# Kernel optimization log

Measured on AMD Instinct MI355X. Metric: run time of the kernel, lower is better.

Reference implementation:

```python
import jax, jax.numpy as jnp
import numpy as np
import math

EPS = 1e-8


def _l2_normalize(v, axis=-1, eps=EPS):
    # Matches torch.nn.functional.normalize: v / max(||v||, eps)
    n = jnp.sqrt(jnp.sum(v * v, axis=axis, keepdims=True))
    return v / jnp.maximum(n, eps)


def _gelu_tanh(x):
    c = math.sqrt(2.0 / math.pi)
    return 0.5 * x * (1.0 + jnp.tanh(c * (x + 0.044715 * x * x * x)))


def setup_inputs() -> dict:
    key = jax.random.key(0)
    k1, k2, k3, k4 = jax.random.split(key, 4)
    B, T, D, K = 8, 4096, 2048, 8
    x = jax.random.normal(k1, (B, T, D), dtype=jnp.float32)
    # module initializes prototypes as normalized randn(K, D)
    P = jax.random.normal(k2, (K, D), dtype=jnp.float32)
    P = _l2_normalize(P)
    log_tau = jnp.asarray(math.log(2.0), dtype=jnp.float32)
    log_blend = jnp.asarray(math.log(0.3 / 0.7), dtype=jnp.float32)
    return {"x": x, "prototypes": P, "log_tau": log_tau, "log_blend": log_blend}


def reference(x, prototypes, log_tau, log_blend):
    tau = jnp.exp(log_tau)
    alpha = jax.nn.sigmoid(log_blend)
    B, T, D = x.shape
    x_norm = _l2_normalize(x)                      # (B, T, D)
    p_norm = _l2_normalize(prototypes)             # (K, D)
    sims = jnp.einsum('btd,kd->btk', x_norm, p_norm)  # tiny K=8 matmul
    sims = jnp.clip(sims, -1.0, 1.0)
    min_dist = jnp.min(1.0 - sims, axis=-1)        # (B, T)
    min_dist = jnp.clip(min_dist, 0.0, 2.0)
    novelty = 1.0 - jnp.exp(-tau * min_dist)       # (B, T)
    scale = 1.0 - alpha + alpha * novelty[..., None]
    scale = jnp.clip(scale, 0.1, 10.0)
    return _gelu_tanh(x * scale)
```

## Files before the change

### kernel.cpp

```cpp
#include <hip/hip_runtime.h>
#include <math.h>

#define D 2048
#define K 8
#define BLOCK 256
#define ROWS 2

typedef __fp16 h2 __attribute__((ext_vector_type(2)));

__device__ __forceinline__ float rcp_fast(float x) {
    return __builtin_amdgcn_rcpf(x);
}

#if __has_builtin(__builtin_amdgcn_fdot2)
#define FDOT2(a, b, c) __builtin_amdgcn_fdot2((a), (b), (c), false)
#else
__device__ __forceinline__ float fdot2_emul(h2 a, h2 b, float c) {
    return fmaf((float)a[0], (float)b[0], fmaf((float)a[1], (float)b[1], c));
}
#define FDOT2 fdot2_emul
#endif

__device__ __forceinline__ float gelu_tanh_fast(float y) {
    const float nc = -2.3022078977f;
    float w = y * fmaf(0.044715f, y * y, 1.0f);
    return y * rcp_fast(1.0f + exp2f(nc * w));
}

__device__ __forceinline__ float dot4(const float4& a, const float4& b) {
    return fmaf(a.w, b.w, fmaf(a.z, b.z, fmaf(a.y, b.y, a.x * b.x)));
}

#define FOLDSTEP(x, y, m)                                   \
    {                                                       \
        float _k = (lane & (m)) ? (y) : (x);                \
        float _o = (lane & (m)) ? (x) : (y);                \
        x = _k + __shfl_xor(_o, (m));                       \
    }

__global__ __launch_bounds__(BLOCK, 4)
void novelty_gelu_kernel(const float* __restrict__ x,
                         const float* __restrict__ P,
                         const float* __restrict__ plog_tau,
                         const float* __restrict__ plog_blend,
                         float* __restrict__ out,
                         int nrows)
{
    __shared__ float s_inv[K];
    __shared__ float redT[2][ROWS][12][4];

    const int tid  = threadIdx.x;
    const int wave = tid >> 6;
    const int lane = tid & 63;
    const int col  = tid * 8;

    for (int k = wave; k < K; k += 4) {
        const float* pr = P + k * D;
        float s = 0.f;
        #pragma unroll
        for (int j = 0; j < 8; ++j) {
            float4 p = *(const float4*)(pr + j * 256 + lane * 4);
            s += dot4(p, p);
        }
        #pragma unroll
        for (int m = 1; m < 64; m <<= 1) s += __shfl_xor(s, m);
        if (lane == 0) s_inv[k] = 1.0f / fmaxf(sqrtf(s), 1e-8f);
    }
    __syncthreads();

    h2 pf[K][4];
    #pragma unroll
    for (int k = 0; k < K; ++k) {
        const float inv = s_inv[k];
        float4 p0 = *(const float4*)(P + k * D + col);
        float4 p1 = *(const float4*)(P + k * D + col + 4);
        pf[k][0] = __builtin_amdgcn_cvt_pkrtz(p0.x * inv, p0.y * inv);
        pf[k][1] = __builtin_amdgcn_cvt_pkrtz(p0.z * inv, p0.w * inv);
        pf[k][2] = __builtin_amdgcn_cvt_pkrtz(p1.x * inv, p1.y * inv);
        pf[k][3] = __builtin_amdgcn_cvt_pkrtz(p1.z * inv, p1.w * inv);
    }

    const float tau   = __expf(plog_tau[0]);
    const float alpha = 1.0f / (1.0f + __expf(-plog_blend[0]));
    const float oma   = 1.0f - alpha;

    const int stride = gridDim.x * ROWS;
    int row = blockIdx.x * ROWS;
    int buf = 0;

    float4 a[ROWS][2], b[ROWS][2];
    if (row < nrows) {
        #pragma unroll
        for (int r = 0; r < ROWS; ++r) {
            const float* xr = x + (size_t)(row + r) * D + col;
            a[r][0] = *(const float4*)(xr);
            a[r][1] = *(const float4*)(xr + 4);
        }
    }

    while (row < nrows) {
        const int nr = row + stride;
        if (nr < nrows) {
            #pragma unroll
            for (int r = 0; r < ROWS; ++r) {
                const float* xn = x + (size_t)(nr + r) * D + col;
                b[r][0] = *(const float4*)(xn);
                b[r][1] = *(const float4*)(xn + 4);
            }
        }

        #pragma unroll
        for (int r = 0; r < ROWS; ++r) {
            h2 xh[4];
            xh[0] = __builtin_amdgcn_cvt_pkrtz(a[r][0].x, a[r][0].y);
            xh[1] = __builtin_amdgcn_cvt_pkrtz(a[r][0].z, a[r][0].w);
            xh[2] = __builtin_amdgcn_cvt_pkrtz(a[r][1].x, a[r][1].y);
            xh[3] = __builtin_amdgcn_cvt_pkrtz(a[r][1].z, a[r][1].w);

            float ssq = 0.f;
            float dt[K];
            #pragma unroll
            for (int k = 0; k < K; ++k) dt[k] = 0.f;
            #pragma unroll
            for (int i = 0; i < 4; ++i) {
                ssq = FDOT2(xh[i], xh[i], ssq);
                #pragma unroll
                for (int k = 0; k < K; ++k)
                    dt[k] = FDOT2(xh[i], pf[k][i], dt[k]);
            }

            FOLDSTEP(dt[0], dt[1], 1);
            FOLDSTEP(dt[2], dt[3], 1);
            FOLDSTEP(dt[4], dt[5], 1);
            FOLDSTEP(dt[6], dt[7], 1);
            FOLDSTEP(dt[0], dt[2], 2);
            FOLDSTEP(dt[4], dt[6], 2);
            FOLDSTEP(dt[0], dt[4], 4);
            float vd = dt[0];
            vd += __shfl_xor(vd, 8);
            vd += __shfl_xor(vd, 16);
            vd += __shfl_xor(vd, 32);

            #pragma unroll
            for (int m = 1; m < 64; m <<= 1) ssq += __shfl_xor(ssq, m);

            if (lane < 8)       redT[buf][r][lane][wave] = vd;
            else if (lane == 8) redT[buf][r][8][wave]    = ssq;
        }

        __syncthreads();

        #pragma unroll
        for (int r = 0; r < ROWS; ++r) {
            float4 qs = *(const float4*)&redT[buf][r][8][0];
            float tssq = (qs.x + qs.y) + (qs.z + qs.w);
            float dmax = -3.0e38f;
            #pragma unroll
            for (int k = 0; k < K; ++k) {
                float4 q = *(const float4*)&redT[buf][r][k][0];
                dmax = fmaxf(dmax, (q.x + q.y) + (q.z + q.w));
            }
            const float inv_nx = 1.0f / fmaxf(sqrtf(tssq), 1e-8f);
            float sim = fminf(1.0f, fmaxf(-1.0f, dmax * inv_nx));
            float md  = fminf(fmaxf(1.0f - sim, 0.0f), 2.0f);
            float scale = oma + alpha * (1.0f - __expf(-tau * md));
            scale = fminf(fmaxf(scale, 0.1f), 10.0f);

            float* outr = out + (size_t)(row + r) * D + col;
            float4 o0, o1;
            o0.x = gelu_tanh_fast(a[r][0].x * scale);
            o0.y = gelu_tanh_fast(a[r][0].y * scale);
            o0.z = gelu_tanh_fast(a[r][0].z * scale);
            o0.w = gelu_tanh_fast(a[r][0].w * scale);
            o1.x = gelu_tanh_fast(a[r][1].x * scale);
            o1.y = gelu_tanh_fast(a[r][1].y * scale);
            o1.z = gelu_tanh_fast(a[r][1].z * scale);
            o1.w = gelu_tanh_fast(a[r][1].w * scale);
            *(float4*)(outr)     = o0;
            *(float4*)(outr + 4) = o1;
        }

        #pragma unroll
        for (int r = 0; r < ROWS; ++r) { a[r][0] = b[r][0]; a[r][1] = b[r][1]; }
        row = nr;
        buf ^= 1;
    }
}

extern "C" void kernel_launch(void* const* d_in, const int* in_sizes, int n_in,
                              void* d_out, int out_size, void* d_ws, size_t ws_size,
                              hipStream_t stream) {
    const float* x  = (const float*)d_in[0];
    const float* P  = (const float*)d_in[1];
    const float* lt = (const float*)d_in[2];
    const float* lb = (const float*)d_in[3];
    float* out = (float*)d_out;

    const int nrows = in_sizes[0] / D;
    int grid = nrows / ROWS;
    if (grid > 2048) grid = 2048;

    novelty_gelu_kernel<<<grid, BLOCK, 0, stream>>>(x, P, lt, lb, out, nrows);
}
```

Baseline: 116.4 us.

## Split prototype norm into prelaunch kernel and use one-shot blocks per row pair

Prototype inverse norms move into a separate small kernel that writes to workspace. The persistent grid-stride loop with register double-buffering becomes a one-shot kernel launching one block per two rows. The final GELU now reads x from its fp16-packed copy instead of the fp32 values, so the input is rounded before the activation. This removes the per-block prototype norm recomputation and the loop overhead, but adds a second kernel launch, 16384 blocks that each reload the prototypes, and a loss of output precision.

Result: slower. 158.6 us (+36.3%).

```diff
diff --git a/kernel.cpp b/kernel.cpp
--- a/kernel.cpp
+++ b/kernel.cpp
@@ -39,151 +39,142 @@
     }
 
 __global__ __launch_bounds__(BLOCK, 4)
-void novelty_gelu_kernel(const float* __restrict__ x,
-                         const float* __restrict__ P,
-                         const float* __restrict__ plog_tau,
-                         const float* __restrict__ plog_blend,
-                         float* __restrict__ out,
-                         int nrows)
+void proto_norm_kernel(const float* __restrict__ P, float* __restrict__ invn)
 {
-    __shared__ float s_inv[K];
-    __shared__ float redT[2][ROWS][12][4];
+    __shared__ float part[4];
+    const int k    = blockIdx.x;
+    const int tid  = threadIdx.x;
+    const int wave = tid >> 6;
+    const int lane = tid & 63;
+
+    const float* pr = P + (size_t)k * D + tid * 8;
+    float4 p0 = *(const float4*)pr;
+    float4 p1 = *(const float4*)(pr + 4);
+    float s = dot4(p0, p0) + dot4(p1, p1);
+    #pragma unroll
+    for (int m = 1; m < 64; m <<= 1) s += __shfl_xor(s, m);
+    if (lane == 0) part[wave] = s;
+    __syncthreads();
+    if (tid == 0) {
+        float t = part[0] + part[1] + part[2] + part[3];
+        invn[k] = 1.0f / fmaxf(sqrtf(t), 1e-8f);
+    }
+}
+
+__global__ __launch_bounds__(BLOCK, 4)
+void novelty_gelu_oneshot(const float* __restrict__ x,
+                          const float* __restrict__ P,
+                          const float* __restrict__ invn,
+                          const float* __restrict__ plog_tau,
+                          const float* __restrict__ plog_blend,
+                          float* __restrict__ out,
+                          int nrows)
+{
+    __shared__ float redT[ROWS][9][4];
+    __shared__ float s_scale[ROWS];
 
     const int tid  = threadIdx.x;
     const int wave = tid >> 6;
     const int lane = tid & 63;
     const int col  = tid * 8;
+    const int r0   = blockIdx.x * ROWS;
 
-    for (int k = wave; k < K; k += 4) {
-        const float* pr = P + k * D;
-        float s = 0.f;
-        #pragma unroll
-        for (int j = 0; j < 8; ++j) {
-            float4 p = *(const float4*)(pr + j * 256 + lane * 4);
-            s += dot4(p, p);
-        }
-        #pragma unroll
-        for (int m = 1; m < 64; m <<= 1) s += __shfl_xor(s, m);
-        if (lane == 0) s_inv[k] = 1.0f / fmaxf(sqrtf(s), 1e-8f);
+    h2 xh[ROWS][4];
+    #pragma unroll
+    for (int r = 0; r < ROWS; ++r) {
+        const float* xr = x + (size_t)(r0 + r) * D + col;
+        float4 v0 = *(const float4*)(xr);
+        float4 v1 = *(const float4*)(xr + 4);
+        xh[r][0] = __builtin_amdgcn_cvt_pkrtz(v0.x, v0.y);
+        xh[r][1] = __builtin_amdgcn_cvt_pkrtz(v0.z, v0.w);
+        xh[r][2] = __builtin_amdgcn_cvt_pkrtz(v1.x, v1.y);
+        xh[r][3] = __builtin_amdgcn_cvt_pkrtz(v1.z, v1.w);
     }
-    __syncthreads();
 
     h2 pf[K][4];
     #pragma unroll
     for (int k = 0; k < K; ++k) {
-        const float inv = s_inv[k];
-        float4 p0 = *(const float4*)(P + k * D + col);
-        float4 p1 = *(const float4*)(P + k * D + col + 4);
+        const float inv = invn[k];
+        float4 p0 = *(const float4*)(P + (size_t)k * D + col);
+        float4 p1 = *(const float4*)(P + (size_t)k * D + col + 4);
         pf[k][0] = __builtin_amdgcn_cvt_pkrtz(p0.x * inv, p0.y * inv);
         pf[k][1] = __builtin_amdgcn_cvt_pkrtz(p0.z * inv, p0.w * inv);
         pf[k][2] = __builtin_amdgcn_cvt_pkrtz(p1.x * inv, p1.y * inv);
         pf[k][3] = __builtin_amdgcn_cvt_pkrtz(p1.z * inv, p1.w * inv);
     }
 
-    const float tau   = __expf(plog_tau[0]);
-    const float alpha = 1.0f / (1.0f + __expf(-plog_blend[0]));
-    const float oma   = 1.0f - alpha;
+    #pragma unroll
+    for (int r = 0; r < ROWS; ++r) {
+        float ssq = 0.f;
+        float dt[K];
+        #pragma unroll
+        for (int k = 0; k < K; ++k) dt[k] = 0.f;
+        #pragma unroll
+        for (int i = 0; i < 4; ++i) {
+            ssq = FDOT2(xh[r][i], xh[r][i], ssq);
+            #pragma unroll
+            for (int k = 0; k < K; ++k)
+                dt[k] = FDOT2(xh[r][i], pf[k][i], dt[k]);
+        }
 
-    const int stride = gridDim.x * ROWS;
-    int row = blockIdx.x * ROWS;
-    int buf = 0;
+        FOLDSTEP(dt[0], dt[1], 1);
+        FOLDSTEP(dt[2], dt[3], 1);
+        FOLDSTEP(dt[4], dt[5], 1);
+        FOLDSTEP(dt[6], dt[7], 1);
+        FOLDSTEP(dt[0], dt[2], 2);
+        FOLDSTEP(dt[4], dt[6], 2);
+        FOLDSTEP(dt[0], dt[4], 4);
+        float vd = dt[0];
+        vd += __shfl_xor(vd, 8);
+        vd += __shfl_xor(vd, 16);
+        vd += __shfl_xor(vd, 32);
 
-    float4 a[ROWS][2], b[ROWS][2];
-    if (row < nrows) {
         #pragma unroll
-        for (int r = 0; r < ROWS; ++r) {
-            const float* xr = x + (size_t)(row + r) * D + col;
-            a[r][0] = *(const float4*)(xr);
-            a[r][1] = *(const float4*)(xr + 4);
-        }
+        for (int m = 1; m < 64; m <<= 1) ssq += __shfl_xor(ssq, m);
+
+        if (lane < 8)       redT[r][lane][wave] = vd;
+        else if (lane == 8) redT[r][8][wave]    = ssq;
     }
 
-    while (row < nrows) {
-        const int nr = row + stride;
-        if (nr < nrows) {
-            #pragma unroll
-            for (int r = 0; r < ROWS; ++r) {
-                const float* xn = x + (size_t)(nr + r) * D + col;
-                b[r][0] = *(const float4*)(xn);
-                b[r][1] = *(const float4*)(xn + 4);
-            }
+    __syncthreads();
+
+    if (wave < ROWS) {
+        const int r = wave;
+        float4 qs = *(const float4*)&redT[r][8][0];
+        float tssq = (qs.x + qs.y) + (qs.z + qs.w);
+        float dmax = -3.0e38f;
+        #pragma unroll
+        for (int k = 0; k < K; ++k) {
+            float4 q = *(const float4*)&redT[r][k][0];
+            dmax = fmaxf(dmax, (q.x + q.y) + (q.z + q.w));
         }
+        const float tau   = __expf(plog_tau[0]);
+        const float alpha = 1.0f / (1.0f + __expf(-plog_blend[0]));
+        const float inv_nx = 1.0f / fmaxf(sqrtf(tssq), 1e-8f);
+        float sim = fminf(1.0f, fmaxf(-1.0f, dmax * inv_nx));
+        float md  = fminf(fmaxf(1.0f - sim, 0.0f), 2.0f);
+        float scale = (1.0f - alpha) + alpha * (1.0f - __expf(-tau * md));
+        scale = fminf(fmaxf(scale, 0.1f), 10.0f);
+        if (lane == 0) s_scale[r] = scale;
+    }
 
-        #pragma unroll
-        for (int r = 0; r < ROWS; ++r) {
-            h2 xh[4];
-            xh[0] = __builtin_amdgcn_cvt_pkrtz(a[r][0].x, a[r][0].y);
-            xh[1] = __builtin_amdgcn_cvt_pkrtz(a[r][0].z, a[r][0].w);
-            xh[2] = __builtin_amdgcn_cvt_pkrtz(a[r][1].x, a[r][1].y);
-            xh[3] = __builtin_amdgcn_cvt_pkrtz(a[r][1].z, a[r][1].w);
+    __syncthreads();
 
-            float ssq = 0.f;
-            float dt[K];
-            #pragma unroll
-            for (int k = 0; k < K; ++k) dt[k] = 0.f;
-            #pragma unroll
-            for (int i = 0; i < 4; ++i) {
-                ssq = FDOT2(xh[i], xh[i], ssq);
-                #pragma unroll
-                for (int k = 0; k < K; ++k)
-                    dt[k] = FDOT2(xh[i], pf[k][i], dt[k]);
-            }
-
-            FOLDSTEP(dt[0], dt[1], 1);
-            FOLDSTEP(dt[2], dt[3], 1);
-            FOLDSTEP(dt[4], dt[5], 1);
-            FOLDSTEP(dt[6], dt[7], 1);
-            FOLDSTEP(dt[0], dt[2], 2);
-            FOLDSTEP(dt[4], dt[6], 2);
-            FOLDSTEP(dt[0], dt[4], 4);
-            float vd = dt[0];
-            vd += __shfl_xor(vd, 8);
-            vd += __shfl_xor(vd, 16);
-            vd += __shfl_xor(vd, 32);
-
-            #pragma unroll
-            for (int m = 1; m < 64; m <<= 1) ssq += __shfl_xor(ssq, m);
-
-            if (lane < 8)       redT[buf][r][lane][wave] = vd;
-            else if (lane == 8) redT[buf][r][8][wave]    = ssq;
-        }
-
-        __syncthreads();
-
-        #pragma unroll
-        for (int r = 0; r < ROWS; ++r) {
-            float4 qs = *(const float4*)&redT[buf][r][8][0];
-            float tssq = (qs.x + qs.y) + (qs.z + qs.w);
-            float dmax = -3.0e38f;
-            #pragma unroll
-            for (int k = 0; k < K; ++k) {
-                float4 q = *(const float4*)&redT[buf][r][k][0];
-                dmax = fmaxf(dmax, (q.x + q.y) + (q.z + q.w));
-            }
-            const float inv_nx = 1.0f / fmaxf(sqrtf(tssq), 1e-8f);
-            float sim = fminf(1.0f, fmaxf(-1.0f, dmax * inv_nx));
-            float md  = fminf(fmaxf(1.0f - sim, 0.0f), 2.0f);
-            float scale = oma + alpha * (1.0f - __expf(-tau * md));
-            scale = fminf(fmaxf(scale, 0.1f), 10.0f);
-
-            float* outr = out + (size_t)(row + r) * D + col;
-            float4 o0, o1;
-            o0.x = gelu_tanh_fast(a[r][0].x * scale);
-            o0.y = gelu_tanh_fast(a[r][0].y * scale);
-            o0.z = gelu_tanh_fast(a[r][0].z * scale);
-            o0.w = gelu_tanh_fast(a[r][0].w * scale);
-            o1.x = gelu_tanh_fast(a[r][1].x * scale);
-            o1.y = gelu_tanh_fast(a[r][1].y * scale);
-            o1.z = gelu_tanh_fast(a[r][1].z * scale);
-            o1.w = gelu_tanh_fast(a[r][1].w * scale);
-            *(float4*)(outr)     = o0;
-            *(float4*)(outr + 4) = o1;
-        }
-
-        #pragma unroll
-        for (int r = 0; r < ROWS; ++r) { a[r][0] = b[r][0]; a[r][1] = b[r][1]; }
-        row = nr;
-        buf ^= 1;
+    #pragma unroll
+    for (int r = 0; r < ROWS; ++r) {
+        const float sc = s_scale[r];
+        float* outr = out + (size_t)(r0 + r) * D + col;
+        float4 o0, o1;
+        o0.x = gelu_tanh_fast((float)xh[r][0][0] * sc);
+        o0.y = gelu_tanh_fast((float)xh[r][0][1] * sc);
+        o0.z = gelu_tanh_fast((float)xh[r][1][0] * sc);
+        o0.w = gelu_tanh_fast((float)xh[r][1][1] * sc);
+        o1.x = gelu_tanh_fast((float)xh[r][2][0] * sc);
+        o1.y = gelu_tanh_fast((float)xh[r][2][1] * sc);
+        o1.z = gelu_tanh_fast((float)xh[r][3][0] * sc);
+        o1.w = gelu_tanh_fast((float)xh[r][3][1] * sc);
+        *(float4*)(outr)     = o0;
+        *(float4*)(outr + 4) = o1;
     }
 }
 
@@ -194,11 +185,11 @@
     const float* P  = (const float*)d_in[1];
     const float* lt = (const float*)d_in[2];
     const float* lb = (const float*)d_in[3];
-    float* out = (float*)d_out;
+    float* out  = (float*)d_out;
+    float* invn = (float*)d_ws;
 
     const int nrows = in_sizes[0] / D;
-    int grid = nrows / ROWS;
-    if (grid > 2048) grid = 2048;
 
-    novelty_gelu_kernel<<<grid, BLOCK, 0, stream>>>(x, P, lt, lb, out, nrows);
+    proto_norm_kernel<<<K, BLOCK, 0, stream>>>(P, invn);
+    novelty_gelu_oneshot<<<nrows / ROWS, BLOCK, 0, stream>>>(x, P, invn, lt, lb, out, nrows);
 }
```
